# Kernel optimization log

Hardware: AMD Instinct MI355X
Metric: run time of the kernel (lower is better)

The kernel has to match this reference:

```python
import jax, jax.numpy as jnp
import numpy as np
from jax import lax

DN = ('NCHW', 'OIHW', 'NCHW')

def _dwsep(x, dw, pw_w, pw_b, stride):
    # depthwise: groups = in_channels, kernel (C,1,3,3)
    y = lax.conv_general_dilated(x, dw, (stride, stride), [(1, 1), (1, 1)],
                                 dimension_numbers=DN, feature_group_count=x.shape[1])
    # pointwise 1x1
    y = lax.conv_general_dilated(y, pw_w, (1, 1), 'VALID', dimension_numbers=DN)
    return y + pw_b[None, :, None, None]

def setup_inputs() -> dict:
    key = jax.random.key(0)
    ks = jax.random.split(key, 16)
    s = 0.1
    inp = {
        'flow_raw': jax.random.normal(ks[0], (32, 2, 480, 640), jnp.float32),
        'dw1': jax.random.normal(ks[1], (5, 1, 3, 3), jnp.float32) * s,
        'pw1_w': jax.random.normal(ks[2], (32, 5, 1, 1), jnp.float32) * s,
        'pw1_b': jnp.zeros((32,), jnp.float32),
        'dw2': jax.random.normal(ks[3], (32, 1, 3, 3), jnp.float32) * s,
        'pw2_w': jax.random.normal(ks[4], (64, 32, 1, 1), jnp.float32) * s,
        'pw2_b': jnp.zeros((64,), jnp.float32),
        'dw3': jax.random.normal(ks[5], (64, 1, 3, 3), jnp.float32) * s,
        'pw3_w': jax.random.normal(ks[6], (64, 64, 1, 1), jnp.float32) * s,
        'pw3_b': jnp.zeros((64,), jnp.float32),
        'attn_w': jax.random.normal(ks[7], (1, 64, 1, 1), jnp.float32) * s,
        'attn_b': jnp.zeros((1,), jnp.float32),
        'mlp1_w': jax.random.normal(ks[8], (32, 64), jnp.float32) * s,
        'mlp1_b': jnp.zeros((32,), jnp.float32),
        'mlp2_w': jax.random.normal(ks[9], (3, 32), jnp.float32) * s,
        'mlp2_b': jnp.zeros((3,), jnp.float32),
        'w_ih': jax.random.normal(ks[10], (96, 3), jnp.float32) * s,
        'w_hh': jax.random.normal(ks[11], (96, 32), jnp.float32) * s,
        'b_ih': jnp.zeros((96,), jnp.float32),
        'b_hh': jnp.zeros((96,), jnp.float32),
        'fc_w': jnp.zeros((3, 32), jnp.float32),  # gru_fc init to zero in torch code
        'fc_b': jnp.zeros((3,), jnp.float32),
    }
    return inp

def reference(flow_raw, dw1, pw1_w, pw1_b, dw2, pw2_w, pw2_b, dw3, pw3_w, pw3_b,
              attn_w, attn_b, mlp1_w, mlp1_b, mlp2_w, mlp2_b,
              w_ih, w_hh, b_ih, b_hh, fc_w, fc_b):
    B, _, H, W = flow_raw.shape
    # coordinate channels (x, y, r^2)
    y = jnp.linspace(-1.0, 1.0, H)
    x = jnp.linspace(-1.0, 1.0, W)
    yy, xx = jnp.meshgrid(y, x, indexing='ij')
    coords = jnp.stack([xx, yy, xx**2 + yy**2], axis=0)            # (3,H,W)
    coords_b = jnp.broadcast_to(coords[None], (B, 3, H, W))
    inp = jnp.concatenate([flow_raw, coords_b], axis=1)            # (B,5,H,W)

    f = jax.nn.elu(_dwsep(inp, dw1, pw1_w, pw1_b, 2))              # (B,32,H/2,W/2)
    f = jax.nn.elu(_dwsep(f, dw2, pw2_w, pw2_b, 2))                # (B,64,H/4,W/4)
    f = jax.nn.elu(_dwsep(f, dw3, pw3_w, pw3_b, 2))                # (B,64,H/8,W/8)

    # attention pooling
    logits = jnp.einsum('bchw,oc->bohw', f, attn_w[:, :, 0, 0]) + attn_b[None, :, None, None]
    Bs, _, Hs, Ws = logits.shape
    w = jax.nn.softmax(logits.reshape(Bs, Hs * Ws), axis=-1)       # (B, HW)
    pooled = jnp.einsum('bcn,bn->bc', f.reshape(Bs, 64, Hs * Ws), w)  # (B,64)

    # omega MLP
    h1 = jax.nn.elu(pooled @ mlp1_w.T + mlp1_b)
    omega_inst = h1 @ mlp2_w.T + mlp2_b                            # (B,3)

    # single-step GRU, h0 = 0 (PyTorch gate order: r, z, n)
    h0 = jnp.zeros((B, 32), flow_raw.dtype)
    gi = omega_inst @ w_ih.T + b_ih                                # (B,96)
    gh = h0 @ w_hh.T + b_hh
    i_r, i_z, i_n = jnp.split(gi, 3, axis=-1)
    h_r, h_z, h_n = jnp.split(gh, 3, axis=-1)
    r = jax.nn.sigmoid(i_r + h_r)
    z = jax.nn.sigmoid(i_z + h_z)
    n = jnp.tanh(i_n + r * h_n)
    h = (1.0 - z) * n + z * h0                                     # (B,32)

    delta_omega = h @ fc_w.T + fc_b
    return omega_inst + delta_omega
```

## Files before the change

### kernel.cpp

```cpp
#include <hip/hip_runtime.h>
#include <hip/hip_bf16.h>

#define H0 480
#define W0 640
#define H1 240
#define W1 320
#define H2 120
#define W2 160
#define H3 60
#define W3 80

#define W_PW1T  0
#define W_PW2T  160
#define W_PW3T  2208
#define WBUF_BYTES 65536

#define F2_PB (64 * H2 * W2)
#define F3_PB (64 * H3 * W3)

__global__ __launch_bounds__(256) void k_cvt(
    const float* __restrict__ pw1, const float* __restrict__ pw2,
    const float* __restrict__ pw3, float* __restrict__ wb)
{
    int t = threadIdx.x;
    for (int i = t; i < 160;  i += 256) { int o = i / 5,  c = i % 5;  wb[W_PW1T + c*32 + o] = pw1[i]; }
    for (int i = t; i < 2048; i += 256) { int o = i >> 5, c = i & 31; wb[W_PW2T + c*64 + o] = pw2[i]; }
    for (int i = t; i < 4096; i += 256) { int o = i >> 6, c = i & 63; wb[W_PW3T + c*64 + o] = pw3[i]; }
}

__global__ __launch_bounds__(256, 3) void k_fuse12(
    const float* __restrict__ flow, const float* __restrict__ dw1,
    const float* __restrict__ b1, const float* __restrict__ dw2,
    const float* __restrict__ b2, const float* __restrict__ wb,
    float* __restrict__ out)
{
    int idx = blockIdx.x * 256 + threadIdx.x;
    int ow = idx % W2; int tmp = idx / W2; int oh = tmp % H2; int b = tmp / H2;

    int fh0 = 2*oh - 1, fw0 = 2*ow - 1;
    const float sy = 2.f / (H0 - 1), sx = 2.f / (W0 - 1);

    float d[9][5];
    float vm[9];

    #pragma unroll
    for (int r = 0; r < 3; r++) {
        #pragma unroll
        for (int s = 0; s < 3; s++) {
            int p = r*3 + s;
            int fh = fh0 + r, fw = fw0 + s;
            vm[p] = (fh >= 0 && fw >= 0) ? 1.f : 0.f;
            int fhc = fh < 0 ? 0 : fh, fwc = fw < 0 ? 0 : fw;
            int ih0 = 2*fhc - 1, iw0 = 2*fwc - 1;
            float mh[3] = { ih0 >= 0 ? 1.f : 0.f, 1.f, 1.f };
            float mw[3] = { iw0 >= 0 ? 1.f : 0.f, 1.f, 1.f };
            int ihx[3] = { ih0 < 0 ? 0 : ih0, ih0 + 1, ih0 + 2 };
            int iwx[3] = { iw0 < 0 ? 0 : iw0, iw0 + 1, iw0 + 2 };

            #pragma unroll
            for (int c = 0; c < 2; c++) {
                const float* base = flow + ((size_t)(b*2 + c)) * (H0*W0);
                float a = 0.f;
                #pragma unroll
                for (int ky = 0; ky < 3; ky++) {
                    const float* rp = base + (size_t)ihx[ky] * W0;
                    #pragma unroll
                    for (int kx = 0; kx < 3; kx++)
                        a = fmaf(dw1[c*9 + ky*3 + kx], (mh[ky]*mw[kx]) * rp[iwx[kx]], a);
                }
                d[p][c] = a;
            }
            float ax = 0.f, ay = 0.f, ar = 0.f;
            #pragma unroll
            for (int ky = 0; ky < 3; ky++) {
                float yv = fmaf((float)(ih0 + ky), sy, -1.f);
                #pragma unroll
                for (int kx = 0; kx < 3; kx++) {
                    float xv = fmaf((float)(iw0 + kx), sx, -1.f);
                    float m = mh[ky] * mw[kx];
                    ax = fmaf(dw1[18 + ky*3 + kx], m * xv, ax);
                    ay = fmaf(dw1[27 + ky*3 + kx], m * yv, ay);
                    ar = fmaf(dw1[36 + ky*3 + kx], m * (xv*xv + yv*yv), ar);
                }
            }
            d[p][2] = ax; d[p][3] = ay; d[p][4] = ar;
        }
    }

    float acc[64];
    #pragma unroll
    for (int o = 0; o < 64; o++) acc[o] = b2[o];

    for (int c = 0; c < 32; c++) {
        const float* w1 = wb + W_PW1T + c;
        float w10 = w1[0], w11 = w1[32], w12 = w1[64], w13 = w1[96], w14 = w1[128];
        float bc = b1[c];
        const float* w9 = dw2 + c*9;
        float dv = 0.f;
        #pragma unroll
        for (int p = 0; p < 9; p++) {
            float v = bc;
            v = fmaf(w10, d[p][0], v);
            v = fmaf(w11, d[p][1], v);
            v = fmaf(w12, d[p][2], v);
            v = fmaf(w13, d[p][3], v);
            v = fmaf(w14, d[p][4], v);
            float f1v = v > 0.f ? v : (__expf(v) - 1.f);
            dv = fmaf(w9[p], f1v * vm[p], dv);
        }
        const float* wr = wb + W_PW2T + c*64;
        #pragma unroll
        for (int o = 0; o < 64; o++) acc[o] = fmaf(wr[o], dv, acc[o]);
    }

    size_t obase = ((size_t)b * 64) * (H2*W2) + (size_t)oh*W2 + ow;
    #pragma unroll
    for (int o = 0; o < 64; o++) {
        float v = acc[o];
        out[obase + (size_t)o*(H2*W2)] = v > 0.f ? v : (__expf(v) - 1.f);
    }
}

__global__ __launch_bounds__(256, 4) void k_stage3(
    const float* __restrict__ in, const float* __restrict__ dw3,
    const float* __restrict__ b3, const float* __restrict__ wb,
    float* __restrict__ out)
{
    int idx = blockIdx.x * 256 + threadIdx.x;
    int ow = idx % W3; int tmp = idx / W3; int oh = tmp % H3; int b = tmp / H3;
    int ih0 = 2*oh - 1, iw0 = 2*ow - 1;
    float mh[3] = { ih0 >= 0 ? 1.f : 0.f, 1.f, 1.f };
    float mw[3] = { iw0 >= 0 ? 1.f : 0.f, 1.f, 1.f };
    int ihx[3] = { ih0 < 0 ? 0 : ih0, ih0 + 1, ih0 + 2 };
    int iwx[3] = { iw0 < 0 ? 0 : iw0, iw0 + 1, iw0 + 2 };
    float m9[9];
    int off[9];
    #pragma unroll
    for (int ky = 0; ky < 3; ky++)
        #pragma unroll
        for (int kx = 0; kx < 3; kx++) {
            m9[ky*3 + kx] = mh[ky] * mw[kx];
            off[ky*3 + kx] = ihx[ky]*W2 + iwx[kx];
        }

    float acc[64];
    #pragma unroll
    for (int o = 0; o < 64; o++) acc[o] = b3[o];

    const float* inb = in + (size_t)b * F2_PB;
    for (int c = 0; c < 64; c++) {
        const float* g = inb + (size_t)c * (H2*W2);
        const float* w9 = dw3 + c*9;
        float dv = 0.f;
        #pragma unroll
        for (int p = 0; p < 9; p++)
            dv = fmaf(w9[p], m9[p] * g[off[p]], dv);
        const float* wr = wb + W_PW3T + c*64;
        #pragma unroll
        for (int o = 0; o < 64; o++) acc[o] = fmaf(wr[o], dv, acc[o]);
    }

    size_t obase = ((size_t)b * 64) * (H3*W3) + (size_t)oh*W3 + ow;
    #pragma unroll
    for (int o = 0; o < 64; o++) {
        float v = acc[o];
        out[obase + (size_t)o*(H3*W3)] = v > 0.f ? v : (__expf(v) - 1.f);
    }
}

__global__ __launch_bounds__(1024) void k_head(
    const float* __restrict__ f3,
    const float* __restrict__ attn_w, const float* __restrict__ attn_b,
    const float* __restrict__ mlp1_w, const float* __restrict__ mlp1_b,
    const float* __restrict__ mlp2_w, const float* __restrict__ mlp2_b,
    const float* __restrict__ w_ih, const float* __restrict__ b_ih,
    const float* __restrict__ b_hh,
    const float* __restrict__ fc_w, const float* __restrict__ fc_b,
    float* __restrict__ out)
{
    const int N  = H3 * W3;
    const int N4 = N / 4;
    __shared__ float s_w[H3 * W3];
    __shared__ float s_attn[64];
    __shared__ float s_redm[16];
    __shared__ float s_reds[16];
    __shared__ float s_inv[1];
    __shared__ float s_pooled[64];
    __shared__ float s_h1[32];
    __shared__ float s_om[3];
    __shared__ float s_h[32];

    int t = threadIdx.x, b = blockIdx.x;
    int lane = t & 63, wid = t >> 6;
    if (t < 64) s_attn[t] = attn_w[t];
    __syncthreads();

    const float4* fb4 = (const float4*)(f3 + (size_t)b * F3_PB);
    float ab = attn_b[0];

    float lmax = -1e30f;
    for (int n4 = t; n4 < N4; n4 += 1024) {
        float4 l = make_float4(ab, ab, ab, ab);
        #pragma unroll 8
        for (int c = 0; c < 64; c++) {
            float4 v = fb4[c * N4 + n4];
            float a = s_attn[c];
            l.x = fmaf(a, v.x, l.x); l.y = fmaf(a, v.y, l.y);
            l.z = fmaf(a, v.z, l.z); l.w = fmaf(a, v.w, l.w);
        }
        ((float4*)s_w)[n4] = l;
        lmax = fmaxf(lmax, fmaxf(fmaxf(l.x, l.y), fmaxf(l.z, l.w)));
    }
    #pragma unroll
    for (int off = 32; off; off >>= 1) lmax = fmaxf(lmax, __shfl_down(lmax, off, 64));
    if (lane == 0) s_redm[wid] = lmax;
    __syncthreads();
    {
        float m = s_redm[0];
        #pragma unroll
        for (int i = 1; i < 16; i++) m = fmaxf(m, s_redm[i]);
        lmax = m;
    }

    float lsum = 0.f;
    for (int n = t; n < N; n += 1024) { float e = __expf(s_w[n] - lmax); s_w[n] = e; lsum += e; }
    #pragma unroll
    for (int off = 32; off; off >>= 1) lsum += __shfl_down(lsum, off, 64);
    if (lane == 0) s_reds[wid] = lsum;
    __syncthreads();
    if (t == 0) {
        float s = 0.f;
        #pragma unroll
        for (int i = 0; i < 16; i++) s += s_reds[i];
        s_inv[0] = 1.f / s;
    }
    __syncthreads();
    float invS = s_inv[0];

    const float4* sw4 = (const float4*)s_w;
    for (int c = wid; c < 64; c += 16) {
        float s = 0.f;
        for (int i = lane; i < N4; i += 64) {
            float4 v = fb4[c * N4 + i];
            float4 w = sw4[i];
            s = fmaf(v.x, w.x, s); s = fmaf(v.y, w.y, s);
            s = fmaf(v.z, w.z, s); s = fmaf(v.w, w.w, s);
        }
        #pragma unroll
        for (int off = 32; off; off >>= 1) s += __shfl_down(s, off, 64);
        if (lane == 0) s_pooled[c] = s * invS;
    }
    __syncthreads();

    if (t < 32) {
        float a = mlp1_b[t];
        #pragma unroll 8
        for (int c = 0; c < 64; c++) a = fmaf(mlp1_w[t*64 + c], s_pooled[c], a);
        s_h1[t] = a > 0.f ? a : (__expf(a) - 1.f);
    }
    __syncthreads();
    if (t < 3) {
        float a = mlp2_b[t];
        for (int j = 0; j < 32; j++) a = fmaf(mlp2_w[t*32 + j], s_h1[j], a);
        s_om[t] = a;
    }
    __syncthreads();
    if (t < 32) {
        float gr = b_ih[t], gz = b_ih[32 + t], gn = b_ih[64 + t];
        #pragma unroll
        for (int k = 0; k < 3; k++) {
            float ok = s_om[k];
            gr = fmaf(w_ih[t*3 + k],        ok, gr);
            gz = fmaf(w_ih[(32 + t)*3 + k], ok, gz);
            gn = fmaf(w_ih[(64 + t)*3 + k], ok, gn);
        }
        float hr = b_hh[t], hz = b_hh[32 + t], hn = b_hh[64 + t];
        float r = 1.f / (1.f + __expf(-(gr + hr)));
        float z = 1.f / (1.f + __expf(-(gz + hz)));
        float nn = tanhf(gn + r * hn);
        s_h[t] = (1.f - z) * nn;
    }
    __syncthreads();
    if (t < 3) {
        float dl = fc_b[t];
        for (int j = 0; j < 32; j++) dl = fmaf(fc_w[t*32 + j], s_h[j], dl);
        out[b*3 + t] = s_om[t] + dl;
    }
}

extern "C" void kernel_launch(void* const* d_in, const int* in_sizes, int n_in,
                              void* d_out, int out_size, void* d_ws, size_t ws_size,
                              hipStream_t stream)
{
    const float* flow = (const float*)d_in[0];
    float* wb = (float*)d_ws;

    float* f2 = (float*)((char*)d_ws + WBUF_BYTES);
    float* f3 = f2 + (size_t)32 * F2_PB;

    k_cvt<<<1, 256, 0, stream>>>(
        (const float*)d_in[2], (const float*)d_in[5], (const float*)d_in[8], wb);

    k_fuse12<<<(32*H2*W2)/256, 256, 0, stream>>>(
        flow, (const float*)d_in[1], (const float*)d_in[3],
        (const float*)d_in[4], (const float*)d_in[6], wb, f2);

    k_stage3<<<(32*H3*W3)/256, 256, 0, stream>>>(
        f2, (const float*)d_in[7], (const float*)d_in[9], wb, f3);

    k_head<<<32, 1024, 0, stream>>>(f3,
        (const float*)d_in[10], (const float*)d_in[11],
        (const float*)d_in[12], (const float*)d_in[13],
        (const float*)d_in[14], (const float*)d_in[15],
        (const float*)d_in[16], (const float*)d_in[18],
        (const float*)d_in[19], (const float*)d_in[20],
        (const float*)d_in[21], (float*)d_out);
}
```

Before: 344.8 us.

## Split stage3 output channels across thread halves and vectorize stencil loads

Stage3 now assigns each pixel to two threads, each computing 32 of the 64 output channels, which doubles the grid and halves per-thread accumulators; the launch bound goes from 4 to 6 blocks per SM. Both the fused stage1/2 and stage3 kernels load the right two stencil taps as one float2 and apply the boundary mask once per row, and the accumulators and weight reads use float2. This aims to raise occupancy and cut load instructions, at the cost of each depthwise 3x3 tap being computed twice in stage3. The float2 loads at iw0+1 are 8-byte aligned only because iw0 is odd.

```diff
diff --git a/kernel.cpp b/kernel.cpp
--- a/kernel.cpp
+++ b/kernel.cpp
@@ -52,44 +52,53 @@
             vm[p] = (fh >= 0 && fw >= 0) ? 1.f : 0.f;
             int fhc = fh < 0 ? 0 : fh, fwc = fw < 0 ? 0 : fw;
             int ih0 = 2*fhc - 1, iw0 = 2*fwc - 1;
-            float mh[3] = { ih0 >= 0 ? 1.f : 0.f, 1.f, 1.f };
-            float mw[3] = { iw0 >= 0 ? 1.f : 0.f, 1.f, 1.f };
-            int ihx[3] = { ih0 < 0 ? 0 : ih0, ih0 + 1, ih0 + 2 };
-            int iwx[3] = { iw0 < 0 ? 0 : iw0, iw0 + 1, iw0 + 2 };
+            float mh0 = ih0 >= 0 ? 1.f : 0.f;
+            float mw0 = iw0 >= 0 ? 1.f : 0.f;
+            int ihw[3] = { ih0 < 0 ? 0 : ih0, ih0 + 1, ih0 + 2 };
+            int iwc = iw0 < 0 ? 0 : iw0;
 
             #pragma unroll
             for (int c = 0; c < 2; c++) {
                 const float* base = flow + ((size_t)(b*2 + c)) * (H0*W0);
+                const float* w9 = dw1 + c*9;
                 float a = 0.f;
                 #pragma unroll
                 for (int ky = 0; ky < 3; ky++) {
-                    const float* rp = base + (size_t)ihx[ky] * W0;
-                    #pragma unroll
-                    for (int kx = 0; kx < 3; kx++)
-                        a = fmaf(dw1[c*9 + ky*3 + kx], (mh[ky]*mw[kx]) * rp[iwx[kx]], a);
+                    const float* rp = base + (size_t)ihw[ky] * W0;
+                    float  t0  = rp[iwc];
+                    float2 t12 = *(const float2*)(rp + iw0 + 1);
+                    float rowv = w9[ky*3 + 0] * (mw0 * t0);
+                    rowv = fmaf(w9[ky*3 + 1], t12.x, rowv);
+                    rowv = fmaf(w9[ky*3 + 2], t12.y, rowv);
+                    a = (ky == 0) ? fmaf(mh0, rowv, a) : (a + rowv);
                 }
                 d[p][c] = a;
             }
-            float ax = 0.f, ay = 0.f, ar = 0.f;
-            #pragma unroll
-            for (int ky = 0; ky < 3; ky++) {
-                float yv = fmaf((float)(ih0 + ky), sy, -1.f);
+            {
+                float mh[3] = { mh0, 1.f, 1.f };
+                float mw[3] = { mw0, 1.f, 1.f };
+                float ax = 0.f, ay = 0.f, ar = 0.f;
                 #pragma unroll
-                for (int kx = 0; kx < 3; kx++) {
-                    float xv = fmaf((float)(iw0 + kx), sx, -1.f);
-                    float m = mh[ky] * mw[kx];
-                    ax = fmaf(dw1[18 + ky*3 + kx], m * xv, ax);
-                    ay = fmaf(dw1[27 + ky*3 + kx], m * yv, ay);
-                    ar = fmaf(dw1[36 + ky*3 + kx], m * (xv*xv + yv*yv), ar);
+                for (int ky = 0; ky < 3; ky++) {
+                    float yv = fmaf((float)(ih0 + ky), sy, -1.f);
+                    #pragma unroll
+                    for (int kx = 0; kx < 3; kx++) {
+                        float xv = fmaf((float)(iw0 + kx), sx, -1.f);
+                        float m = mh[ky] * mw[kx];
+                        ax = fmaf(dw1[18 + ky*3 + kx], m * xv, ax);
+                        ay = fmaf(dw1[27 + ky*3 + kx], m * yv, ay);
+                        ar = fmaf(dw1[36 + ky*3 + kx], m * (xv*xv + yv*yv), ar);
+                    }
                 }
+                d[p][2] = ax; d[p][3] = ay; d[p][4] = ar;
             }
-            d[p][2] = ax; d[p][3] = ay; d[p][4] = ar;
-        }
-    }
-
-    float acc[64];
-    #pragma unroll
-    for (int o = 0; o < 64; o++) acc[o] = b2[o];
+        }
+    }
+
+    float2 acc[32];
+    const float2* b22 = (const float2*)b2;
+    #pragma unroll
+    for (int o = 0; o < 32; o++) acc[o] = b22[o];
 
     for (int c = 0; c < 32; c++) {
         const float* w1 = wb + W_PW1T + c;
@@ -108,44 +117,42 @@
             float f1v = v > 0.f ? v : (__expf(v) - 1.f);
             dv = fmaf(w9[p], f1v * vm[p], dv);
         }
-        const float* wr = wb + W_PW2T + c*64;
-        #pragma unroll
-        for (int o = 0; o < 64; o++) acc[o] = fmaf(wr[o], dv, acc[o]);
+        const float2* wr = (const float2*)(wb + W_PW2T + c*64);
+        #pragma unroll
+        for (int o = 0; o < 32; o++) {
+            acc[o].x = fmaf(wr[o].x, dv, acc[o].x);
+            acc[o].y = fmaf(wr[o].y, dv, acc[o].y);
+        }
     }
 
     size_t obase = ((size_t)b * 64) * (H2*W2) + (size_t)oh*W2 + ow;
     #pragma unroll
-    for (int o = 0; o < 64; o++) {
-        float v = acc[o];
-        out[obase + (size_t)o*(H2*W2)] = v > 0.f ? v : (__expf(v) - 1.f);
-    }
-}
-
-__global__ __launch_bounds__(256, 4) void k_stage3(
+    for (int o = 0; o < 32; o++) {
+        float vx = acc[o].x, vy = acc[o].y;
+        out[obase + (size_t)(2*o  )*(H2*W2)] = vx > 0.f ? vx : (__expf(vx) - 1.f);
+        out[obase + (size_t)(2*o+1)*(H2*W2)] = vy > 0.f ? vy : (__expf(vy) - 1.f);
+    }
+}
+
+__global__ __launch_bounds__(256, 6) void k_stage3(
     const float* __restrict__ in, const float* __restrict__ dw3,
     const float* __restrict__ b3, const float* __restrict__ wb,
     float* __restrict__ out)
 {
-    int idx = blockIdx.x * 256 + threadIdx.x;
-    int ow = idx % W3; int tmp = idx / W3; int oh = tmp % H3; int b = tmp / H3;
+    int t = threadIdx.x;
+    int px = blockIdx.x * 128 + (t & 127);
+    int half = t >> 7;
+    int ow = px % W3; int tmp = px / W3; int oh = tmp % H3; int b = tmp / H3;
     int ih0 = 2*oh - 1, iw0 = 2*ow - 1;
-    float mh[3] = { ih0 >= 0 ? 1.f : 0.f, 1.f, 1.f };
-    float mw[3] = { iw0 >= 0 ? 1.f : 0.f, 1.f, 1.f };
-    int ihx[3] = { ih0 < 0 ? 0 : ih0, ih0 + 1, ih0 + 2 };
-    int iwx[3] = { iw0 < 0 ? 0 : iw0, iw0 + 1, iw0 + 2 };
-    float m9[9];
-    int off[9];
-    #pragma unroll
-    for (int ky = 0; ky < 3; ky++)
-        #pragma unroll
-        for (int kx = 0; kx < 3; kx++) {
-            m9[ky*3 + kx] = mh[ky] * mw[kx];
-            off[ky*3 + kx] = ihx[ky]*W2 + iwx[kx];
-        }
-
-    float acc[64];
-    #pragma unroll
-    for (int o = 0; o < 64; o++) acc[o] = b3[o];
+    float mh0 = ih0 >= 0 ? 1.f : 0.f;
+    float mw0 = iw0 >= 0 ? 1.f : 0.f;
+    int ihw[3] = { ih0 < 0 ? 0 : ih0, ih0 + 1, ih0 + 2 };
+    int iwc = iw0 < 0 ? 0 : iw0;
+
+    float2 acc[16];
+    const float2* b32 = (const float2*)(b3 + half*32);
+    #pragma unroll
+    for (int o = 0; o < 16; o++) acc[o] = b32[o];
 
     const float* inb = in + (size_t)b * F2_PB;
     for (int c = 0; c < 64; c++) {
@@ -153,18 +160,29 @@
         const float* w9 = dw3 + c*9;
         float dv = 0.f;
         #pragma unroll
-        for (int p = 0; p < 9; p++)
-            dv = fmaf(w9[p], m9[p] * g[off[p]], dv);
-        const float* wr = wb + W_PW3T + c*64;
-        #pragma unroll
-        for (int o = 0; o < 64; o++) acc[o] = fmaf(wr[o], dv, acc[o]);
-    }
-
-    size_t obase = ((size_t)b * 64) * (H3*W3) + (size_t)oh*W3 + ow;
-    #pragma unroll
-    for (int o = 0; o < 64; o++) {
-        float v = acc[o];
-        out[obase + (size_t)o*(H3*W3)] = v > 0.f ? v : (__expf(v) - 1.f);
+        for (int ky = 0; ky < 3; ky++) {
+            const float* rp = g + (size_t)ihw[ky] * W2;
+            float  t0  = rp[iwc];
+            float2 t12 = *(const float2*)(rp + iw0 + 1);
+            float rowv = w9[ky*3 + 0] * (mw0 * t0);
+            rowv = fmaf(w9[ky*3 + 1], t12.x, rowv);
+            rowv = fmaf(w9[ky*3 + 2], t12.y, rowv);
+            dv = (ky == 0) ? fmaf(mh0, rowv, dv) : (dv + rowv);
+        }
+        const float2* wr = (const float2*)(wb + W_PW3T + c*64 + half*32);
+        #pragma unroll
+        for (int o = 0; o < 16; o++) {
+            acc[o].x = fmaf(wr[o].x, dv, acc[o].x);
+            acc[o].y = fmaf(wr[o].y, dv, acc[o].y);
+        }
+    }
+
+    size_t obase = ((size_t)b*64 + half*32) * (H3*W3) + (size_t)oh*W3 + ow;
+    #pragma unroll
+    for (int o = 0; o < 16; o++) {
+        float vx = acc[o].x, vy = acc[o].y;
+        out[obase + (size_t)(2*o  )*(H3*W3)] = vx > 0.f ? vx : (__expf(vx) - 1.f);
+        out[obase + (size_t)(2*o+1)*(H3*W3)] = vy > 0.f ? vy : (__expf(vy) - 1.f);
     }
 }
 
@@ -305,7 +323,7 @@
         flow, (const float*)d_in[1], (const float*)d_in[3],
         (const float*)d_in[4], (const float*)d_in[6], wb, f2);
 
-    k_stage3<<<(32*H3*W3)/256, 256, 0, stream>>>(
+    k_stage3<<<(32*H3*W3*2)/256, 256, 0, stream>>>(
         f2, (const float*)d_in[7], (const float*)d_in[9], wb, f3);
 
     k_head<<<32, 1024, 0, stream>>>(f3,
```

After: 469.8 us. 36.2% more time.
